# Performance work log

Hardware: AMD Instinct MI355X
Metric: run time of the kernel (lower is better)

Reference implementation:

```python
import jax, jax.numpy as jnp
import numpy as np

B, IN, OUT = 65536, 1024, 1024
NB, D, H, L = 16, 32, 64, 4      # n_bundles, bundle_dim, norm_mlp hidden, n_latent_layers
TOT = NB * D                      # total latent dim = 512 (also encoder/decoder hidden)


def setup_inputs() -> dict:
    key = jax.random.key(0)
    ks = jax.random.split(key, 20)
    rn = lambda k, shape, s=0.02: (jax.random.normal(k, shape, dtype=jnp.float32) * s)
    return {
        "x": jax.random.normal(ks[0], (B, IN), dtype=jnp.float32),
        # encoder: Linear(IN,TOT), Linear(TOT,TOT), Linear(TOT,TOT)
        "enc_w1": rn(ks[1], (TOT, IN)), "enc_b1": jnp.zeros((TOT,), jnp.float32),
        "enc_w2": rn(ks[2], (TOT, TOT)), "enc_b2": jnp.zeros((TOT,), jnp.float32),
        "enc_w3": rn(ks[3], (TOT, TOT)), "enc_b3": jnp.zeros((TOT,), jnp.float32),
        # per-latent-layer norm_mlp: Linear(NB,H)+b, Linear(H,H)+b, Linear(H,NB) no bias
        "mlp1_w": rn(ks[4], (L, H, NB)), "mlp1_b": jnp.zeros((L, H), jnp.float32),
        "mlp2_w": rn(ks[5], (L, H, H)),  "mlp2_b": jnp.zeros((L, H), jnp.float32),
        "mlp3_w": rn(ks[6], (L, NB, H)),
        # mixing_weights[i][j] has shape (d_i, d_j); homogeneous -> [L,NB,NB,D,D], init 0.01*randn
        "mix_w": rn(ks[7], (L, NB, NB, D, D), 0.01),
        "gate_bias": jnp.zeros((L, NB), jnp.float32),
        # decoder: Linear(TOT,TOT), Linear(TOT,TOT), Linear(TOT,OUT)
        "dec_w1": rn(ks[8], (TOT, TOT)), "dec_b1": jnp.zeros((TOT,), jnp.float32),
        "dec_w2": rn(ks[9], (TOT, TOT)), "dec_b2": jnp.zeros((TOT,), jnp.float32),
        "dec_w3": rn(ks[10], (OUT, TOT)), "dec_b3": jnp.zeros((OUT,), jnp.float32),
    }


def _gelu(v):
    return jax.nn.gelu(v, approximate=False)  # torch nn.GELU default (erf)


def _soft_equivariant(z, m1w, m1b, m2w, m2b, m3w, mw, gb):
    # z: [B, TOT] -> bundles [B, NB, D] (homogeneous dims, contiguous split == reshape)
    zb = z.reshape(z.shape[0], NB, D)
    norms = jnp.linalg.norm(zb, axis=-1) + 1e-8          # [B, NB]
    h = _gelu(norms @ m1w.T + m1b)                        # [B, H]
    h = _gelu(h @ m2w.T + m2b)                            # [B, H]
    scales = jax.nn.softplus(h @ m3w.T)                   # [B, NB]
    equi = zb * scales[:, :, None]                        # [B, NB, D]
    # mixed_i = sum_j F.linear(bundles[j], W[i][j]) = bundles[j] @ W[i][j].T
    mixed = jnp.einsum('bjd,ijed->bie', zb, mw)           # [B, NB, D]
    gates = jax.nn.sigmoid(gb)                            # [NB]
    combined = equi + gates[None, :, None] * mixed        # [B, NB, D]
    return z + combined.reshape(z.shape[0], TOT)          # residual


def reference(x, enc_w1, enc_b1, enc_w2, enc_b2, enc_w3, enc_b3,
              mlp1_w, mlp1_b, mlp2_w, mlp2_b, mlp3_w, mix_w, gate_bias,
              dec_w1, dec_b1, dec_w2, dec_b2, dec_w3, dec_b3):
    # encoder
    z = _gelu(x @ enc_w1.T + enc_b1)
    z = _gelu(z @ enc_w2.T + enc_b2)
    z = z @ enc_w3.T + enc_b3
    # latent dynamics: L SoftEquivariantLayers (fixed small loop over layers)
    for l in range(L):
        z = _soft_equivariant(z, mlp1_w[l], mlp1_b[l], mlp2_w[l], mlp2_b[l],
                              mlp3_w[l], mix_w[l], gate_bias[l])
    # decoder
    y = _gelu(z @ dec_w1.T + dec_b1)
    y = _gelu(y @ dec_w2.T + dec_b2)
    return y @ dec_w3.T + dec_b3
```

## Files before the change

### kernel.cpp

```cpp
#include <hip/hip_runtime.h>
#include <hip/hip_bf16.h>

typedef float f32x4 __attribute__((ext_vector_type(4)));
typedef __bf16 bf16x8 __attribute__((ext_vector_type(8)));
typedef unsigned short u16x8 __attribute__((ext_vector_type(8)));
typedef unsigned short u16;

__device__ __forceinline__ u16 f2bf(float f) {
  __bf16 h = (__bf16)f;
  return __builtin_bit_cast(u16, h);
}
__device__ __forceinline__ float bf2f(u16 s) {
  return __uint_as_float(((unsigned int)s) << 16);
}
__device__ __forceinline__ float gelu_f(float x) {
  return 0.5f * x * (1.0f + erff(x * 0.70710678118654752f));
}
__device__ __forceinline__ void gload_lds16(const void* g, void* l) {
  __builtin_amdgcn_global_load_lds((const __attribute__((address_space(1))) void*)g,
                                   (__attribute__((address_space(3))) void*)l, 16, 0, 0);
}
#define MFMA(a, b, c) __builtin_amdgcn_mfma_f32_16x16x32_bf16((a), (b), (c), 0, 0, 0)
#define BARRIER_PINNED() do { \
    __builtin_amdgcn_s_barrier(); \
    asm volatile("" ::: "memory"); \
    __builtin_amdgcn_sched_barrier(0); \
  } while (0)

__global__ void cvt_all(const float* __restrict__ e1, const float* __restrict__ e2,
                        const float* __restrict__ e3, const float* __restrict__ d1,
                        const float* __restrict__ d2, const float* __restrict__ d3,
                        const float* __restrict__ mx, u16* __restrict__ dst)
{
  int i = blockIdx.x * blockDim.x + threadIdx.x;
  int stride = gridDim.x * blockDim.x;
  for (; i < 3145728; i += stride) {
    float v;
    if (i < 524288)        v = e1[i];
    else if (i < 786432)   v = e2[i - 524288];
    else if (i < 1048576)  v = e3[i - 786432];
    else if (i < 1310720)  v = d1[i - 1048576];
    else if (i < 1572864)  v = d2[i - 1310720];
    else if (i < 2097152)  v = d3[i - 1572864];
    else {
      int j = i - 2097152;
      int l = j >> 18, rem = j & 262143;
      int o = rem >> 9, k = rem & 511;
      int bi = o >> 5, e = o & 31, jj = k >> 5, dd = k & 31;
      v = mx[(((l * 16 + bi) * 16 + jj) * 32 + e) * 32 + dd];
    }
    dst[i] = f2bf(v);
  }
}

__global__ void cvt_x(const float* __restrict__ s, u16* __restrict__ d) {
  int i = blockIdx.x * blockDim.x + threadIdx.x;
  int stride = gridDim.x * blockDim.x;
  for (; i < 8388608; i += stride) {
    float4 v0 = *(const float4*)(s + (size_t)i * 8);
    float4 v1 = *(const float4*)(s + (size_t)i * 8 + 4);
    u16x8 u;
    u[0] = f2bf(v0.x); u[1] = f2bf(v0.y); u[2] = f2bf(v0.z); u[3] = f2bf(v0.w);
    u[4] = f2bf(v1.x); u[5] = f2bf(v1.y); u[6] = f2bf(v1.z); u[7] = f2bf(v1.w);
    *(u16x8*)(d + (size_t)i * 8) = u;
  }
}

template<int EPI>
__global__ __launch_bounds__(512, 2)
void gemm_wide(const u16* __restrict__ A, const u16* __restrict__ Bw,
               const float* __restrict__ bias, void* __restrict__ Cp,
               const u16* __restrict__ zOld, const float* __restrict__ scales,
               const float* __restrict__ gateBias, int N, int nOff, int K)
{
  extern __shared__ char smem[];
  const int tid = threadIdx.x;
  const int lane = tid & 63;
  const int wid = tid >> 6;
  const int m0 = blockIdx.x << 6;

  const int r16 = lane & 15;
  const int kg = (lane >> 4) << 3;
  const int sw = (r16 & 7) << 4;

  const int NT = K >> 6;
  f32x4 acc[4][4] = {};

  auto stage = [&](int kt, int b) {
    {
      int c = tid;
      int row = c >> 3;
      int cb = (c & 7) << 4;
      const char* g = (const char*)(A + (size_t)(m0 + row) * K + (kt << 6))
                      + (cb ^ ((row & 7) << 4));
      gload_lds16(g, smem + (b << 13) + (wid << 10));
    }
    #pragma unroll
    for (int p = 0; p < 8; ++p) {
      int c = (p << 9) + tid;
      int row = c >> 3;
      int cb = (c & 7) << 4;
      const char* g = (const char*)(Bw + (size_t)(nOff + row) * K + (kt << 6))
                      + (cb ^ ((row & 7) << 4));
      gload_lds16(g, smem + 16384 + (b << 16) + (((p << 3) + wid) << 10));
    }
  };

  stage(0, 0);
  asm volatile("s_waitcnt vmcnt(0)" ::: "memory");
  BARRIER_PINNED();

  for (int kt = 0; kt < NT; ++kt) {
    const int cur = kt & 1;
    if (kt + 1 < NT) stage(kt + 1, cur ^ 1);

    const char* Ac = smem + (cur << 13);
    const char* Bc = smem + 16384 + (cur << 16);
    #pragma unroll
    for (int kk = 0; kk < 64; kk += 32) {
      const int kb = ((kk + kg) << 1) ^ sw;
      bf16x8 av[4], bv[4];
      #pragma unroll
      for (int m = 0; m < 4; ++m)
        av[m] = *(const bf16x8*)(Ac + (m * 16 + r16) * 128 + kb);
      #pragma unroll
      for (int n = 0; n < 4; ++n)
        bv[n] = *(const bf16x8*)(Bc + ((wid << 6) + n * 16 + r16) * 128 + kb);
      __builtin_amdgcn_s_setprio(1);
      #pragma unroll
      for (int m = 0; m < 4; ++m)
        #pragma unroll
        for (int n = 0; n < 4; ++n)
          acc[m][n] = MFMA(av[m], bv[n], acc[m][n]);
      __builtin_amdgcn_s_setprio(0);
    }
    asm volatile("s_waitcnt vmcnt(0)" ::: "memory");
    BARRIER_PINNED();
  }

  const int colBase = nOff + (wid << 6) + r16;
  const int rowBase = m0 + ((lane >> 4) << 2);
  #pragma unroll
  for (int n = 0; n < 4; ++n) {
    const int col = colBase + n * 16;
    float bv_ = 0.f, gate = 0.f;
    if constexpr (EPI == 0 || EPI == 1 || EPI == 3) bv_ = bias[col];
    if constexpr (EPI == 2) gate = 1.f / (1.f + expf(-gateBias[(col - nOff) >> 5]));
    #pragma unroll
    for (int m = 0; m < 4; ++m) {
      #pragma unroll
      for (int r = 0; r < 4; ++r) {
        const int row = rowBase + m * 16 + r;
        float v = acc[m][n][r];
        if constexpr (EPI == 0) {
          ((u16*)Cp)[(size_t)row * N + col] = f2bf(gelu_f(v + bv_));
        } else if constexpr (EPI == 1) {
          ((u16*)Cp)[(size_t)row * N + col] = f2bf(v + bv_);
        } else if constexpr (EPI == 2) {
          float sc = scales[(size_t)row * 16 + ((col - nOff) >> 5)];
          float zo = bf2f(zOld[(size_t)row * 512 + (col - nOff)]);
          ((u16*)Cp)[(size_t)row * N + col] = f2bf(zo * (1.f + sc) + gate * v);
        } else {
          ((float*)Cp)[(size_t)row * N + col] = v + bv_;
        }
      }
    }
  }
}

__global__ __launch_bounds__(256, 2)
void norm_mlp2(const u16* __restrict__ z,
               const float* __restrict__ w1, const float* __restrict__ b1,
               const float* __restrict__ w2, const float* __restrict__ b2,
               const float* __restrict__ w3, float* __restrict__ scales)
{
  __shared__ float nrm[256][17];
  const int tid = threadIdx.x;
  const size_t base = (size_t)blockIdx.x << 8;

  #pragma unroll
  for (int p = 0; p < 16; ++p) {
    const int C = (p << 8) + tid;
    const int r = C >> 4, b = C & 15;
    const u16* zp = z + ((base + r) << 9) + (b << 5);
    float ss = 0.f;
    #pragma unroll
    for (int q = 0; q < 4; ++q) {
      u16x8 v = *(const u16x8*)(zp + q * 8);
      #pragma unroll
      for (int j = 0; j < 8; ++j) { float f = bf2f(v[j]); ss += f * f; }
    }
    nrm[r][b] = sqrtf(ss) + 1e-8f;
  }
  __syncthreads();

  float nr[16];
  #pragma unroll
  for (int i = 0; i < 16; ++i) nr[i] = nrm[tid][i];

  float h2[64];
  #pragma unroll
  for (int j = 0; j < 64; ++j) h2[j] = b2[j];

  for (int kt = 0; kt < 4; ++kt) {
    float h1t[16];
    #pragma unroll
    for (int k16 = 0; k16 < 16; ++k16) {
      const int k = (kt << 4) + k16;
      float t = b1[k];
      #pragma unroll
      for (int i = 0; i < 16; ++i) t += nr[i] * w1[k * 16 + i];
      h1t[k16] = gelu_f(t);
    }
    const float* w2t = w2 + (kt << 4);
    #pragma unroll
    for (int j = 0; j < 64; ++j) {
      float s = 0.f;
      #pragma unroll
      for (int k16 = 0; k16 < 16; ++k16) s += h1t[k16] * w2t[j * 64 + k16];
      h2[j] += s;
    }
  }
  #pragma unroll
  for (int j = 0; j < 64; ++j) h2[j] = gelu_f(h2[j]);

  float* srow = scales + ((base + tid) << 4);
  #pragma unroll
  for (int b = 0; b < 16; ++b) {
    float s = 0.f;
    #pragma unroll
    for (int k = 0; k < 64; ++k) s += h2[k] * w3[b * 64 + k];
    s = (s > 20.f) ? s : log1pf(expf(s));
    srow[b] = s;
  }
}

#define WIDE_SMEM 147456

extern "C" void kernel_launch(void* const* d_in, const int* in_sizes, int n_in,
                              void* d_out, int out_size, void* d_ws, size_t ws_size,
                              hipStream_t stream)
{
  (void)in_sizes; (void)n_in; (void)out_size; (void)ws_size;
  const float* x      = (const float*)d_in[0];
  const float* enc_w1 = (const float*)d_in[1];
  const float* enc_b1 = (const float*)d_in[2];
  const float* enc_w2 = (const float*)d_in[3];
  const float* enc_b2 = (const float*)d_in[4];
  const float* enc_w3 = (const float*)d_in[5];
  const float* enc_b3 = (const float*)d_in[6];
  const float* mlp1_w = (const float*)d_in[7];
  const float* mlp1_b = (const float*)d_in[8];
  const float* mlp2_w = (const float*)d_in[9];
  const float* mlp2_b = (const float*)d_in[10];
  const float* mlp3_w = (const float*)d_in[11];
  const float* mix_w  = (const float*)d_in[12];
  const float* gate_b = (const float*)d_in[13];
  const float* dec_w1 = (const float*)d_in[14];
  const float* dec_b1 = (const float*)d_in[15];
  const float* dec_w2 = (const float*)d_in[16];
  const float* dec_b2 = (const float*)d_in[17];
  const float* dec_w3 = (const float*)d_in[18];
  const float* dec_b3 = (const float*)d_in[19];

  char* ws = (char*)d_ws;
  const int M = 65536;

  u16*   xb     = (u16*)ws;
  u16*   zA     = (u16*)(ws + 134217728ULL);
  u16*   zB     = (u16*)ws;
  float* scales = (float*)(ws + 201326592ULL);
  u16*   wBase  = (u16*)(ws + 205520896ULL);
  u16* wE1 = wBase;
  u16* wE2 = wE1 + 524288;
  u16* wE3 = wE2 + 262144;
  u16* wD1 = wE3 + 262144;
  u16* wD2 = wD1 + 262144;
  u16* wD3 = wD2 + 262144;
  u16* wMix = wD3 + 524288;

  hipError_t e;
  e = hipFuncSetAttribute(reinterpret_cast<const void*>(&gemm_wide<0>),
                          hipFuncAttributeMaxDynamicSharedMemorySize, WIDE_SMEM);
  e = hipFuncSetAttribute(reinterpret_cast<const void*>(&gemm_wide<1>),
                          hipFuncAttributeMaxDynamicSharedMemorySize, WIDE_SMEM);
  e = hipFuncSetAttribute(reinterpret_cast<const void*>(&gemm_wide<2>),
                          hipFuncAttributeMaxDynamicSharedMemorySize, WIDE_SMEM);
  e = hipFuncSetAttribute(reinterpret_cast<const void*>(&gemm_wide<3>),
                          hipFuncAttributeMaxDynamicSharedMemorySize, WIDE_SMEM);
  (void)e;

  cvt_all<<<512, 256, 0, stream>>>(enc_w1, enc_w2, enc_w3, dec_w1, dec_w2, dec_w3,
                                   mix_w, wBase);

  dim3 blk(512);
  const int grid = 1024;

  cvt_x<<<2048, 256, 0, stream>>>(x, xb);
  gemm_wide<0><<<grid, blk, WIDE_SMEM, stream>>>(xb, wE1, enc_b1, zA, nullptr, nullptr, nullptr, 512, 0, 1024);
  gemm_wide<0><<<grid, blk, WIDE_SMEM, stream>>>(zA, wE2, enc_b2, zB, nullptr, nullptr, nullptr, 512, 0, 512);
  gemm_wide<1><<<grid, blk, WIDE_SMEM, stream>>>(zB, wE3, enc_b3, zA, nullptr, nullptr, nullptr, 512, 0, 512);

  u16* cur = zA;
  u16* nxt = zB;
  for (int l = 0; l < 4; ++l) {
    norm_mlp2<<<256, dim3(256), 0, stream>>>(cur, mlp1_w + l * 1024, mlp1_b + l * 64,
                                             mlp2_w + l * 4096, mlp2_b + l * 64,
                                             mlp3_w + l * 1024, scales);
    gemm_wide<2><<<grid, blk, WIDE_SMEM, stream>>>(cur, wMix + (size_t)l * 262144, nullptr, nxt,
                                                   cur, scales, gate_b + l * 16, 512, 0, 512);
    u16* t = cur; cur = nxt; nxt = t;
  }

  gemm_wide<0><<<grid, blk, WIDE_SMEM, stream>>>(cur, wD1, dec_b1, nxt, nullptr, nullptr, nullptr, 512, 0, 512);
  { u16* t = cur; cur = nxt; nxt = t; }
  gemm_wide<0><<<grid, blk, WIDE_SMEM, stream>>>(cur, wD2, dec_b2, nxt, nullptr, nullptr, nullptr, 512, 0, 512);
  { u16* t = cur; cur = nxt; nxt = t; }
  gemm_wide<3><<<grid, blk, WIDE_SMEM, stream>>>(cur, wD3, dec_b3, d_out, nullptr, nullptr, nullptr, 1024, 0, 512);
  gemm_wide<3><<<grid, blk, WIDE_SMEM, stream>>>(cur, wD3, dec_b3, d_out, nullptr, nullptr, nullptr, 1024, 512, 512);
}
```

Baseline: 1.403 ms.

## Retile GEMMs to 256x128 blocks with triple-buffered LDS and XCD-aware block mapping

Replaces the 64x512 block tile with a 256x128 tile computed by a 2x4 warp grid, where each warp owns 128x32 outputs. Loading moves to a three-stage LDS ring with partial vmcnt waits, so two tiles are in flight. Block indices are remapped so each XCD works on a contiguous M range, and the final decoder layer runs as one launch instead of two. The aim is better load balance and deeper prefetch overlap, at the cost of more A-side LDS traffic per MFMA and altered L2 reuse of the weights.

```diff
diff --git a/kernel.cpp b/kernel.cpp
--- a/kernel.cpp
+++ b/kernel.cpp
@@ -68,86 +68,113 @@
 
 template<int EPI>
 __global__ __launch_bounds__(512, 2)
-void gemm_wide(const u16* __restrict__ A, const u16* __restrict__ Bw,
-               const float* __restrict__ bias, void* __restrict__ Cp,
-               const u16* __restrict__ zOld, const float* __restrict__ scales,
-               const float* __restrict__ gateBias, int N, int nOff, int K)
+void gemm_big(const u16* __restrict__ A, const u16* __restrict__ Bw,
+              const float* __restrict__ bias, void* __restrict__ Cp,
+              const u16* __restrict__ zOld, const float* __restrict__ scales,
+              const float* __restrict__ gateBias, int M, int N, int K)
 {
   extern __shared__ char smem[];
   const int tid = threadIdx.x;
   const int lane = tid & 63;
   const int wid = tid >> 6;
-  const int m0 = blockIdx.x << 6;
-
+
+  const int nx = N >> 7;
+  const int ny = M >> 8;
+  const int d = blockIdx.x;
+  const int xcd = d & 7;
+  const int seq = d >> 3;
+  const int by = xcd * (ny >> 3) + seq / nx;
+  const int bx = seq - (seq / nx) * nx;
+  const int m0 = by << 8;
+  const int n0 = bx << 7;
+
+  const int wr = wid >> 2;
+  const int wc = wid & 3;
   const int r16 = lane & 15;
   const int kg = (lane >> 4) << 3;
   const int sw = (r16 & 7) << 4;
 
+  const u16* pA[4];
+  const u16* pB[2];
+  #pragma unroll
+  for (int it = 0; it < 4; ++it) {
+    int c = ((it * 8 + wid) << 6) + lane;
+    int row = c >> 3;
+    int cb = (c & 7) << 4;
+    pA[it] = A + (size_t)(m0 + row) * K + ((cb ^ ((row & 7) << 4)) >> 1);
+  }
+  #pragma unroll
+  for (int it = 0; it < 2; ++it) {
+    int c = ((it * 8 + wid) << 6) + lane;
+    int row = c >> 3;
+    int cb = (c & 7) << 4;
+    pB[it] = Bw + (size_t)(n0 + row) * K + ((cb ^ ((row & 7) << 4)) >> 1);
+  }
+
+  auto stage = [&](int kt, int b) {
+    char* dstA = smem + b * 49152;
+    char* dstB = dstA + 32768;
+    const int ko = kt << 6;
+    #pragma unroll
+    for (int it = 0; it < 4; ++it)
+      gload_lds16(pA[it] + ko, dstA + ((it * 8 + wid) << 10));
+    #pragma unroll
+    for (int it = 0; it < 2; ++it)
+      gload_lds16(pB[it] + ko, dstB + ((it * 8 + wid) << 10));
+  };
+
   const int NT = K >> 6;
-  f32x4 acc[4][4] = {};
-
-  auto stage = [&](int kt, int b) {
-    {
-      int c = tid;
-      int row = c >> 3;
-      int cb = (c & 7) << 4;
-      const char* g = (const char*)(A + (size_t)(m0 + row) * K + (kt << 6))
-                      + (cb ^ ((row & 7) << 4));
-      gload_lds16(g, smem + (b << 13) + (wid << 10));
-    }
-    #pragma unroll
-    for (int p = 0; p < 8; ++p) {
-      int c = (p << 9) + tid;
-      int row = c >> 3;
-      int cb = (c & 7) << 4;
-      const char* g = (const char*)(Bw + (size_t)(nOff + row) * K + (kt << 6))
-                      + (cb ^ ((row & 7) << 4));
-      gload_lds16(g, smem + 16384 + (b << 16) + (((p << 3) + wid) << 10));
-    }
-  };
+  f32x4 acc[8][2] = {};
 
   stage(0, 0);
-  asm volatile("s_waitcnt vmcnt(0)" ::: "memory");
-  BARRIER_PINNED();
-
+  stage(1, 1);
+
+  int cb = 0, ib = 2;
   for (int kt = 0; kt < NT; ++kt) {
-    const int cur = kt & 1;
-    if (kt + 1 < NT) stage(kt + 1, cur ^ 1);
-
-    const char* Ac = smem + (cur << 13);
-    const char* Bc = smem + 16384 + (cur << 16);
+    if (kt + 1 < NT) { asm volatile("s_waitcnt vmcnt(6)" ::: "memory"); }
+    else             { asm volatile("s_waitcnt vmcnt(0)" ::: "memory"); }
+    BARRIER_PINNED();
+
+    if (kt + 2 < NT) {
+      stage(kt + 2, ib);
+      ib = (ib == 2) ? 0 : ib + 1;
+    }
+
+    const char* Ac = smem + cb * 49152;
+    const char* Bc = Ac + 32768;
     #pragma unroll
     for (int kk = 0; kk < 64; kk += 32) {
       const int kb = ((kk + kg) << 1) ^ sw;
-      bf16x8 av[4], bv[4];
-      #pragma unroll
-      for (int m = 0; m < 4; ++m)
-        av[m] = *(const bf16x8*)(Ac + (m * 16 + r16) * 128 + kb);
-      #pragma unroll
-      for (int n = 0; n < 4; ++n)
-        bv[n] = *(const bf16x8*)(Bc + ((wid << 6) + n * 16 + r16) * 128 + kb);
-      __builtin_amdgcn_s_setprio(1);
-      #pragma unroll
-      for (int m = 0; m < 4; ++m)
+      bf16x8 bv0 = *(const bf16x8*)(Bc + ((wc * 32 + r16) << 7) + kb);
+      bf16x8 bv1 = *(const bf16x8*)(Bc + ((wc * 32 + 16 + r16) << 7) + kb);
+      #pragma unroll
+      for (int mh = 0; mh < 2; ++mh) {
+        bf16x8 av[4];
         #pragma unroll
-        for (int n = 0; n < 4; ++n)
-          acc[m][n] = MFMA(av[m], bv[n], acc[m][n]);
-      __builtin_amdgcn_s_setprio(0);
-    }
-    asm volatile("s_waitcnt vmcnt(0)" ::: "memory");
-    BARRIER_PINNED();
-  }
-
-  const int colBase = nOff + (wid << 6) + r16;
-  const int rowBase = m0 + ((lane >> 4) << 2);
-  #pragma unroll
-  for (int n = 0; n < 4; ++n) {
+        for (int m = 0; m < 4; ++m)
+          av[m] = *(const bf16x8*)(Ac + ((wr * 128 + mh * 64 + m * 16 + r16) << 7) + kb);
+        __builtin_amdgcn_s_setprio(1);
+        #pragma unroll
+        for (int m = 0; m < 4; ++m) {
+          acc[mh * 4 + m][0] = MFMA(av[m], bv0, acc[mh * 4 + m][0]);
+          acc[mh * 4 + m][1] = MFMA(av[m], bv1, acc[mh * 4 + m][1]);
+        }
+        __builtin_amdgcn_s_setprio(0);
+      }
+    }
+    cb = (cb == 2) ? 0 : cb + 1;
+  }
+
+  const int colBase = n0 + wc * 32 + r16;
+  const int rowBase = m0 + wr * 128 + ((lane >> 4) << 2);
+  #pragma unroll
+  for (int n = 0; n < 2; ++n) {
     const int col = colBase + n * 16;
     float bv_ = 0.f, gate = 0.f;
     if constexpr (EPI == 0 || EPI == 1 || EPI == 3) bv_ = bias[col];
-    if constexpr (EPI == 2) gate = 1.f / (1.f + expf(-gateBias[(col - nOff) >> 5]));
-    #pragma unroll
-    for (int m = 0; m < 4; ++m) {
+    if constexpr (EPI == 2) gate = 1.f / (1.f + expf(-gateBias[col >> 5]));
+    #pragma unroll
+    for (int m = 0; m < 8; ++m) {
       #pragma unroll
       for (int r = 0; r < 4; ++r) {
         const int row = rowBase + m * 16 + r;
@@ -157,8 +184,8 @@
         } else if constexpr (EPI == 1) {
           ((u16*)Cp)[(size_t)row * N + col] = f2bf(v + bv_);
         } else if constexpr (EPI == 2) {
-          float sc = scales[(size_t)row * 16 + ((col - nOff) >> 5)];
-          float zo = bf2f(zOld[(size_t)row * 512 + (col - nOff)]);
+          float sc = scales[(size_t)row * 16 + (col >> 5)];
+          float zo = bf2f(zOld[(size_t)row * 512 + col]);
           ((u16*)Cp)[(size_t)row * N + col] = f2bf(zo * (1.f + sc) + gate * v);
         } else {
           ((float*)Cp)[(size_t)row * N + col] = v + bv_;
@@ -235,7 +262,7 @@
   }
 }
 
-#define WIDE_SMEM 147456
+#define BIG_SMEM 147456
 
 extern "C" void kernel_launch(void* const* d_in, const int* in_sizes, int n_in,
                               void* d_out, int out_size, void* d_ws, size_t ws_size,
@@ -280,26 +307,27 @@
   u16* wMix = wD3 + 524288;
 
   hipError_t e;
-  e = hipFuncSetAttribute(reinterpret_cast<const void*>(&gemm_wide<0>),
-                          hipFuncAttributeMaxDynamicSharedMemorySize, WIDE_SMEM);
-  e = hipFuncSetAttribute(reinterpret_cast<const void*>(&gemm_wide<1>),
-                          hipFuncAttributeMaxDynamicSharedMemorySize, WIDE_SMEM);
-  e = hipFuncSetAttribute(reinterpret_cast<const void*>(&gemm_wide<2>),
-                          hipFuncAttributeMaxDynamicSharedMemorySize, WIDE_SMEM);
-  e = hipFuncSetAttribute(reinterpret_cast<const void*>(&gemm_wide<3>),
-                          hipFuncAttributeMaxDynamicSharedMemorySize, WIDE_SMEM);
+  e = hipFuncSetAttribute(reinterpret_cast<const void*>(&gemm_big<0>),
+                          hipFuncAttributeMaxDynamicSharedMemorySize, BIG_SMEM);
+  e = hipFuncSetAttribute(reinterpret_cast<const void*>(&gemm_big<1>),
+                          hipFuncAttributeMaxDynamicSharedMemorySize, BIG_SMEM);
+  e = hipFuncSetAttribute(reinterpret_cast<const void*>(&gemm_big<2>),
+                          hipFuncAttributeMaxDynamicSharedMemorySize, BIG_SMEM);
+  e = hipFuncSetAttribute(reinterpret_cast<const void*>(&gemm_big<3>),
+                          hipFuncAttributeMaxDynamicSharedMemorySize, BIG_SMEM);
   (void)e;
 
   cvt_all<<<512, 256, 0, stream>>>(enc_w1, enc_w2, enc_w3, dec_w1, dec_w2, dec_w3,
                                    mix_w, wBase);
 
   dim3 blk(512);
-  const int grid = 1024;
+  const int g512  = 256 * 4;
+  const int g1024 = 256 * 8;
 
   cvt_x<<<2048, 256, 0, stream>>>(x, xb);
-  gemm_wide<0><<<grid, blk, WIDE_SMEM, stream>>>(xb, wE1, enc_b1, zA, nullptr, nullptr, nullptr, 512, 0, 1024);
-  gemm_wide<0><<<grid, blk, WIDE_SMEM, stream>>>(zA, wE2, enc_b2, zB, nullptr, nullptr, nullptr, 512, 0, 512);
-  gemm_wide<1><<<grid, blk, WIDE_SMEM, stream>>>(zB, wE3, enc_b3, zA, nullptr, nullptr, nullptr, 512, 0, 512);
+  gemm_big<0><<<g512, blk, BIG_SMEM, stream>>>(xb, wE1, enc_b1, zA, nullptr, nullptr, nullptr, M, 512, 1024);
+  gemm_big<0><<<g512, blk, BIG_SMEM, stream>>>(zA, wE2, enc_b2, zB, nullptr, nullptr, nullptr, M, 512, 512);
+  gemm_big<1><<<g512, blk, BIG_SMEM, stream>>>(zB, wE3, enc_b3, zA, nullptr, nullptr, nullptr, M, 512, 512);
 
   u16* cur = zA;
   u16* nxt = zB;
@@ -307,15 +335,14 @@
     norm_mlp2<<<256, dim3(256), 0, stream>>>(cur, mlp1_w + l * 1024, mlp1_b + l * 64,
                                              mlp2_w + l * 4096, mlp2_b + l * 64,
                                              mlp3_w + l * 1024, scales);
-    gemm_wide<2><<<grid, blk, WIDE_SMEM, stream>>>(cur, wMix + (size_t)l * 262144, nullptr, nxt,
-                                                   cur, scales, gate_b + l * 16, 512, 0, 512);
+    gemm_big<2><<<g512, blk, BIG_SMEM, stream>>>(cur, wMix + (size_t)l * 262144, nullptr, nxt,
+                                                 cur, scales, gate_b + l * 16, M, 512, 512);
     u16* t = cur; cur = nxt; nxt = t;
   }
 
-  gemm_wide<0><<<grid, blk, WIDE_SMEM, stream>>>(cur, wD1, dec_b1, nxt, nullptr, nullptr, nullptr, 512, 0, 512);
+  gemm_big<0><<<g512, blk, BIG_SMEM, stream>>>(cur, wD1, dec_b1, nxt, nullptr, nullptr, nullptr, M, 512, 512);
   { u16* t = cur; cur = nxt; nxt = t; }
-  gemm_wide<0><<<grid, blk, WIDE_SMEM, stream>>>(cur, wD2, dec_b2, nxt, nullptr, nullptr, nullptr, 512, 0, 512);
+  gemm_big<0><<<g512, blk, BIG_SMEM, stream>>>(cur, wD2, dec_b2, nxt, nullptr, nullptr, nullptr, M, 512, 512);
   { u16* t = cur; cur = nxt; nxt = t; }
-  gemm_wide<3><<<grid, blk, WIDE_SMEM, stream>>>(cur, wD3, dec_b3, d_out, nullptr, nullptr, nullptr, 1024, 0, 512);
-  gemm_wide<3><<<grid, blk, WIDE_SMEM, stream>>>(cur, wD3, dec_b3, d_out, nullptr, nullptr, nullptr, 1024, 512, 512);
-}
+  gemm_big<3><<<g1024, blk, BIG_SMEM, stream>>>(cur, wD3, dec_b3, d_out, nullptr, nullptr, nullptr, M, 1024, 512);
+}
```

Result: faster. 1.199 ms (-14.5%).
